# Optimization experiments

Measured on AMD Instinct MI355X. Metric: run time of the kernel, lower is better.

Reference implementation:

```python
import jax, jax.numpy as jnp
import numpy as np

K = 15; P = 3; IN_CH = 128; OUT_CH = 128
NQ_LRF = 4; NS_LRF = 4; LRF_CH = IN_CH // NQ_LRF  # 32
KP_EXTENT = 1.2; RADIUS = 2.5
NQ = 10000; NS = 10000; H = 32


def setup_inputs() -> dict:
    key = jax.random.key(0)
    ks = jax.random.split(key, 10)
    return {
        "q_pts": jax.random.normal(ks[0], (NQ, P), jnp.float32),
        "s_pts": jax.random.normal(ks[1], (NS, P), jnp.float32),
        "neighb_inds": jax.random.randint(ks[2], (NQ, H), 0, NS + 1),  # index NS == shadow point
        "x": jax.random.normal(ks[3], (NS, IN_CH), jnp.float32),
        "q_lrf": jax.random.normal(ks[4], (NQ, NQ_LRF, P, P), jnp.float32),
        "s_lrf": jax.random.normal(ks[5], (NS, NS_LRF, P, P), jnp.float32),
        "weights": jax.random.normal(ks[6], (K, 2 * IN_CH, OUT_CH), jnp.float32) * 0.02,
        "kernel_points": jax.random.normal(ks[7], (K, P), jnp.float32) * (RADIUS * 0.3),
        "mlp_w": jax.random.normal(ks[8], (NS_LRF * P * P, LRF_CH), jnp.float32) * 0.1,
        "mlp_b": jnp.zeros((LRF_CH,), jnp.float32),
    }


def _forward(q_pts, s_pts, neighb_inds, x, q_lrf, s_lrf, weights, kernel_points, mlp_w, mlp_b):
    Nq, Hn = neighb_inds.shape
    Ns = s_pts.shape[0]
    # q_lrf is only ever used detached in the torch module; kernel points are non-trainable
    q_lrf_d = jax.lax.stop_gradient(q_lrf)
    kp = jax.lax.stop_gradient(kernel_points)

    # gather neighbor coords (shadow row at +1e6), center on queries
    s_pts_pad = jnp.concatenate([s_pts, jnp.full((1, P), 1e6, s_pts.dtype)], 0)
    neighbors = s_pts_pad[neighb_inds] - q_pts[:, None, :]            # [Nq,H,3]
    # rotate into each query LRF
    aligned = jnp.einsum('nhd,nqde->nqhe', neighbors, q_lrf_d)        # [Nq,nq,H,3]
    sq_d = jnp.sum((aligned[..., None, :] - kp) ** 2, axis=-1)        # [Nq,nq,H,K]

    # aligned neighbor LRFs: q_lrf^T @ s_lrf_neighbor
    s_lrf_pad = jnp.concatenate([s_lrf, jnp.zeros_like(s_lrf[:1])], 0)
    nb_lrf = s_lrf_pad[neighb_inds]                                   # [Nq,H,ns,3,3]
    aligned_lrf = jnp.einsum('nqba,nhsbc->nhqsac', q_lrf_d, nb_lrf)   # [Nq,H,nq,ns,3,3]
    aligned_lrf = aligned_lrf.reshape(Nq, Hn, NQ_LRF, NS_LRF * P * P)
    lrf_feat = aligned_lrf @ mlp_w + mlp_b                            # [Nq,H,nq,lrf_ch]
    mask = (neighb_inds < Ns).astype(lrf_feat.dtype)                  # shadow-neighbor mask
    lrf_feat = lrf_feat * mask[:, :, None, None]

    # linear kernel-point influence
    all_w = jnp.clip(1.0 - jnp.sqrt(sq_d) / KP_EXTENT, 0.0)           # [Nq,nq,H,K]
    all_w = jnp.swapaxes(all_w, 2, 3)                                 # [Nq,nq,K,H]

    # gather neighbor features (zero shadow row), append lrf features
    x_pad = jnp.concatenate([x.reshape(Ns, NQ_LRF, LRF_CH),
                             jnp.zeros((1, NQ_LRF, LRF_CH), x.dtype)], 0)
    nb_x = x_pad[neighb_inds]                                         # [Nq,H,nq,lc]
    nb_x = jnp.concatenate([nb_x, lrf_feat], axis=-1)                 # [Nq,H,nq,2lc]
    nb_x = jnp.swapaxes(nb_x, 1, 2)                                   # [Nq,nq,H,2lc]

    # influence-weighted aggregation over neighbors, then per-kernel matmul
    wf = jnp.matmul(all_w, nb_x)                                      # [Nq,nq,K,2lc]
    wf = jnp.transpose(wf, (2, 0, 1, 3)).reshape(K, Nq, 2 * IN_CH)    # [K,Nq,fdim]
    return jnp.einsum('knf,kfo->no', wf, weights)                     # [Nq,out]


def reference(q_pts, s_pts, neighb_inds, x, q_lrf, s_lrf, weights, kernel_points, mlp_w, mlp_b):
    return _forward(q_pts, s_pts, neighb_inds, x, q_lrf, s_lrf, weights, kernel_points, mlp_w, mlp_b)
```

## Files before the change

kernel.cpp:

```cpp
#include <hip/hip_runtime.h>

#define NQn 10000
#define NSn 10000
#define Hh  32
#define FDIM 3840

typedef _Float16 f16x8 __attribute__((ext_vector_type(8)));
typedef float    f32x4 __attribute__((ext_vector_type(4)));

__device__ __forceinline__ unsigned pack2h(float a, float b) {
  union { _Float16 h; unsigned short u; } ua, ub;
  ua.h = (_Float16)a; ub.h = (_Float16)b;
  return (unsigned)ua.u | ((unsigned)ub.u << 16);
}

__global__ __launch_bounds__(256) void ekp_prep5(
    const float* __restrict__ w, const float* __restrict__ x,
    _Float16* __restrict__ wt, _Float16* __restrict__ xh)
{
  const int b = blockIdx.x, tid = threadIdx.x;
  if (b < 625) {
    size_t base = (size_t)b*2048 + (size_t)tid*8;
    float4 a0 = *reinterpret_cast<const float4*>(x + base);
    float4 a1 = *reinterpret_cast<const float4*>(x + base + 4);
    uint4 o;
    o.x = pack2h(a0.x, a0.y); o.y = pack2h(a0.z, a0.w);
    o.z = pack2h(a1.x, a1.y); o.w = pack2h(a1.z, a1.w);
    *reinterpret_cast<uint4*>(xh + base) = o;
  } else if (b == 625) {
    if (tid < 64)
      reinterpret_cast<unsigned*>(xh + (size_t)NSn*128)[tid] = 0u;
  } else {
    __shared__ _Float16 t[32][34];
    const int tt = b - 626;
    const int k0 = (tt % 120) * 32, n0 = (tt / 120) * 32;
    const int c = tid & 31, r0 = tid >> 5;
    #pragma unroll
    for (int p = 0; p < 4; ++p) {
      int r = r0 + p*8;
      t[c][r] = (_Float16)w[(size_t)(k0 + r)*128 + n0 + c];
    }
    __syncthreads();
    #pragma unroll
    for (int p = 0; p < 4; ++p) {
      int r = r0 + p*8;
      wt[(size_t)(n0 + r)*FDIM + k0 + c] = t[r][c];
    }
  }
}

__global__ __launch_bounds__(256, 5) void ekp_stage1j(
    const float* __restrict__ q_pts, const float* __restrict__ s_pts,
    const int*   __restrict__ nbi,   const unsigned short* __restrict__ xh,
    const float* __restrict__ q_lrf, const float* __restrict__ s_lrf,
    const float* __restrict__ kp,    const float* __restrict__ mlp_w,
    const float* __restrict__ mlp_b, _Float16* __restrict__ wf_out)
{
  const int n = blockIdx.x;
  const int tid = threadIdx.x;
  const int lane = tid & 63;
  const int wv = tid >> 6;
  const int l15 = lane & 15, lg = lane >> 4;

  __shared__ float sQ[36];
  __shared__ float sMB[32];
  __shared__ int   sIdx[32];
  __shared__ int   sIdxX[32];
  __shared__ float sZ[32];
  __shared__ float sNbr[32][3];
  __shared__ alignas(16) _Float16 sLrfA[32][72];
  __shared__ alignas(16) _Float16 sBw2[4][32][72];
  __shared__ alignas(16) _Float16 sWb[4][16][40];
  #define sFtP(q, m) (&sBw2[q][m][0])

  if (tid < 36) sQ[tid]  = q_lrf[(size_t)n*36 + tid];
  if (tid < 32) sMB[tid] = mlp_b[tid];
  if (tid < 32) {
    int idx = nbi[(size_t)n*Hh + tid];
    int sh = (idx >= NSn) ? 1 : 0;
    sZ[tid]    = sh ? 0.f : 1.f;
    sIdx[tid]  = sh ? 0 : idx;
    sIdxX[tid] = idx;
  }
  { unsigned* z = (unsigned*)&sBw2[0][0][0];
    for (int i = tid; i < 4608; i += 256) z[i] = 0u; }
  { unsigned* z = (unsigned*)&sLrfA[0][0];
    for (int i = tid; i < 1152; i += 256) z[i] = 0u; }
  __syncthreads();

  if (tid < 96) {
    int h = tid / 3, d = tid - h*3;
    sNbr[h][d] = sZ[h] * s_pts[(size_t)sIdx[h]*3 + d] - q_pts[(size_t)n*3 + d];
  }
  for (int f4i = tid; f4i < 288; f4i += 256) {
    int row = f4i / 9, c4 = f4i - row*9;
    float4 v = *reinterpret_cast<const float4*>(
        s_lrf + (size_t)sIdx[row]*36 + c4*4);
    float z = sZ[row];
    uint2 pk;
    pk.x = pack2h(z*v.x, z*v.y);
    pk.y = pack2h(z*v.z, z*v.w);
    *reinterpret_cast<uint2*>(&sLrfA[row][c4*4]) = pk;
  }
  #pragma unroll
  for (int it = 0; it < 18; ++it) {
    int i = tid + it*256;
    int q = i / 1152, r = i - q*1152;
    int k = r >> 5, m = r & 31;
    int s = k / 9, bc = k - s*9, b = bc / 3, c = bc - b*3;
    int br = (s*9 + c)*32 + m;
    float acc = sQ[q*9 + b*3 + 0] * mlp_w[br]
              + sQ[q*9 + b*3 + 1] * mlp_w[br + 96]
              + sQ[q*9 + b*3 + 2] * mlp_w[br + 192];
    sBw2[q][m][k] = (_Float16)acc;
  }
  __syncthreads();

  {
    int h = lane & 31, kh = lane >> 5;
    float a0 = 0.f, a1 = 0.f, a2 = 0.f;
    #pragma unroll
    for (int d = 0; d < 3; ++d) {
      float nd = sNbr[h][d];
      a0 += nd * sQ[wv*9 + d*3 + 0];
      a1 += nd * sQ[wv*9 + d*3 + 1];
      a2 += nd * sQ[wv*9 + d*3 + 2];
    }
    float z = sZ[h];
    int k0 = kh * 8, kend = kh ? 15 : 8;
    for (int k = k0; k < kend; ++k) {
      float d0 = a0 - kp[k*3+0];
      float d1 = a1 - kp[k*3+1];
      float d2 = a2 - kp[k*3+2];
      float wgt = 1.f - sqrtf(d0*d0 + d1*d1 + d2*d2) * (1.0f/1.2f);
      sWb[wv][k][h] = (_Float16)(z * fmaxf(wgt, 0.f));
    }
    if (kh) sWb[wv][15][h] = (_Float16)0.f;
  }
  {
    f32x4 fa[2][2];
    #pragma unroll
    for (int i = 0; i < 2; ++i)
      #pragma unroll
      for (int j = 0; j < 2; ++j) fa[i][j] = (f32x4){0.f,0.f,0.f,0.f};
    #pragma unroll
    for (int kc = 0; kc < 2; ++kc) {
      f16x8 af0 = *reinterpret_cast<const f16x8*>(&sLrfA[l15][kc*32 + lg*8]);
      f16x8 af1 = *reinterpret_cast<const f16x8*>(&sLrfA[16 + l15][kc*32 + lg*8]);
      f16x8 bf0 = *reinterpret_cast<const f16x8*>(&sBw2[wv][l15][kc*32 + lg*8]);
      f16x8 bf1 = *reinterpret_cast<const f16x8*>(&sBw2[wv][16 + l15][kc*32 + lg*8]);
      fa[0][0] = __builtin_amdgcn_mfma_f32_16x16x32_f16(af0, bf0, fa[0][0], 0, 0, 0);
      fa[0][1] = __builtin_amdgcn_mfma_f32_16x16x32_f16(af0, bf1, fa[0][1], 0, 0, 0);
      fa[1][0] = __builtin_amdgcn_mfma_f32_16x16x32_f16(af1, bf0, fa[1][0], 0, 0, 0);
      fa[1][1] = __builtin_amdgcn_mfma_f32_16x16x32_f16(af1, bf1, fa[1][1], 0, 0, 0);
    }
    #pragma unroll
    for (int ht = 0; ht < 2; ++ht) {
      int hb = ht*16 + lg*4;
      float z0 = sZ[hb+0], z1 = sZ[hb+1], z2 = sZ[hb+2], z3 = sZ[hb+3];
      #pragma unroll
      for (int mt = 0; mt < 2; ++mt) {
        int m = mt*16 + l15;
        float bias = sMB[m];
        uint2 pk;
        pk.x = pack2h(fmaf(z0, bias, fa[ht][mt][0]), fmaf(z1, bias, fa[ht][mt][1]));
        pk.y = pack2h(fmaf(z2, bias, fa[ht][mt][2]), fmaf(z3, bias, fa[ht][mt][3]));
        *reinterpret_cast<uint2*>(sFtP(wv, m) + hb) = pk;
      }
    }
  }
  __syncthreads();

  {
    f16x8 a = *reinterpret_cast<const f16x8*>(&sWb[wv][l15][lg*8]);
    union { unsigned u[4]; f16x8 v; } B0, B1;
    #pragma unroll
    for (int j = 0; j < 8; j += 2) {
      int h0 = lg*8 + j, h1 = h0 + 1;
      size_t r0 = (size_t)sIdxX[h0]*128 + wv*32 + l15;
      size_t r1 = (size_t)sIdxX[h1]*128 + wv*32 + l15;
      B0.u[j >> 1] = (unsigned)xh[r0]      | ((unsigned)xh[r1]      << 16);
      B1.u[j >> 1] = (unsigned)xh[r0 + 16] | ((unsigned)xh[r1 + 16] << 16);
    }
    f16x8 b2 = *reinterpret_cast<const f16x8*>(sFtP(wv, l15) + lg*8);
    f16x8 b3 = *reinterpret_cast<const f16x8*>(sFtP(wv, 16 + l15) + lg*8);

    _Float16* wp = wf_out + (size_t)n*FDIM + wv*64 + l15;
    f32x4 acc;
    acc = (f32x4){0.f,0.f,0.f,0.f};
    acc = __builtin_amdgcn_mfma_f32_16x16x32_f16(a, B0.v, acc, 0, 0, 0);
    #pragma unroll
    for (int v = 0; v < 4; ++v) { int k = lg*4 + v; if (k < 15) wp[k*256 +  0] = (_Float16)acc[v]; }
    acc = (f32x4){0.f,0.f,0.f,0.f};
    acc = __builtin_amdgcn_mfma_f32_16x16x32_f16(a, B1.v, acc, 0, 0, 0);
    #pragma unroll
    for (int v = 0; v < 4; ++v) { int k = lg*4 + v; if (k < 15) wp[k*256 + 16] = (_Float16)acc[v]; }
    acc = (f32x4){0.f,0.f,0.f,0.f};
    acc = __builtin_amdgcn_mfma_f32_16x16x32_f16(a, b2, acc, 0, 0, 0);
    #pragma unroll
    for (int v = 0; v < 4; ++v) { int k = lg*4 + v; if (k < 15) wp[k*256 + 32] = (_Float16)acc[v]; }
    acc = (f32x4){0.f,0.f,0.f,0.f};
    acc = __builtin_amdgcn_mfma_f32_16x16x32_f16(a, b3, acc, 0, 0, 0);
    #pragma unroll
    for (int v = 0; v < 4; ++v) { int k = lg*4 + v; if (k < 15) wp[k*256 + 48] = (_Float16)acc[v]; }
  }
  #undef sFtP
}

__global__ __launch_bounds__(256, 4) void ekp_gemm3(
    const _Float16* __restrict__ A,
    const _Float16* __restrict__ Bt,
    float* __restrict__ C)
{
  __shared__ alignas(16) _Float16 As[32][72];
  __shared__ alignas(16) _Float16 Bs[128][72];
  const int tid = threadIdx.x, lane = tid & 63, w = tid >> 6;
  const int wr = w >> 1, wc = w & 1;
  const int r0 = blockIdx.x * 32;
  const int l15 = lane & 15, lg = lane >> 4;

  f32x4 acc[4];
  #pragma unroll
  for (int i = 0; i < 4; ++i) acc[i] = (f32x4){0.f,0.f,0.f,0.f};

  const int sr = tid >> 3;
  const int ak = (tid & 7) << 3;
  const _Float16* ap = A  + (size_t)(r0 + sr)*FDIM + ak;
  const _Float16* bp = Bt + (size_t)sr*FDIM + ak;

  for (int kc = 0; kc < FDIM; kc += 64) {
    *reinterpret_cast<f16x8*>(&As[sr][ak]) = *reinterpret_cast<const f16x8*>(ap + kc);
    #pragma unroll
    for (int p = 0; p < 4; ++p)
      *reinterpret_cast<f16x8*>(&Bs[p*32 + sr][ak]) =
        *reinterpret_cast<const f16x8*>(bp + (size_t)p*32*FDIM + kc);
    __syncthreads();
    #pragma unroll
    for (int k2 = 0; k2 < 2; ++k2) {
      const int ko = k2*32 + lg*8;
      f16x8 a = *reinterpret_cast<const f16x8*>(&As[wr*16 + l15][ko]);
      #pragma unroll
      for (int ni = 0; ni < 4; ++ni) {
        f16x8 b = *reinterpret_cast<const f16x8*>(&Bs[wc*64 + ni*16 + l15][ko]);
        acc[ni] = __builtin_amdgcn_mfma_f32_16x16x32_f16(a, b, acc[ni], 0, 0, 0);
      }
    }
    __syncthreads();
  }
  #pragma unroll
  for (int v = 0; v < 4; ++v) {
    int gr = r0 + wr*16 + lg*4 + v;
    if (gr < NQn) {
      #pragma unroll
      for (int ni = 0; ni < 4; ++ni)
        C[(size_t)gr*128 + wc*64 + ni*16 + l15] = acc[ni][v];
    }
  }
}

__global__ __launch_bounds__(256) void ekp_stage1_fused(
    const float* __restrict__ q_pts, const float* __restrict__ s_pts,
    const int*   __restrict__ nbi,   const float* __restrict__ x,
    const float* __restrict__ q_lrf, const float* __restrict__ s_lrf,
    const float* __restrict__ weights, const float* __restrict__ kp,
    const float* __restrict__ mlp_w, const float* __restrict__ mlp_b,
    float* __restrict__ out)
{
  const int n = blockIdx.x;
  const int tid = threadIdx.x;

  __shared__ float sQ[36];
  __shared__ float sKP[45];
  __shared__ float sMW[36][32];
  __shared__ float sMB[32];
  __shared__ int   sIdx[32];
  __shared__ int   sShad[32];
  __shared__ float sNbr[32][3];
  __shared__ float sLrf[32][37];
  __shared__ float sW[4][15][32];
  __shared__ float sNbx[32][4][65];

  if (tid < 36) sQ[tid]  = q_lrf[(size_t)n*36 + tid];
  if (tid < 45) sKP[tid] = kp[tid];
  if (tid < 32) sMB[tid] = mlp_b[tid];
  for (int i = tid; i < 36*32; i += 256) sMW[i >> 5][i & 31] = mlp_w[i];
  if (tid < 32) {
    int idx = nbi[(size_t)n*Hh + tid];
    int sh = (idx >= NSn) ? 1 : 0;
    sShad[tid] = sh;
    sIdx[tid]  = sh ? 0 : idx;
  }
  __syncthreads();

  if (tid < 96) {
    int h = tid / 3, d = tid - h*3;
    float v = sShad[h] ? 0.f : s_pts[(size_t)sIdx[h]*3 + d];
    sNbr[h][d] = v - q_pts[(size_t)n*3 + d];
  }
  {
    int h = tid >> 3, j0 = tid & 7;
    const float* src = s_lrf + (size_t)sIdx[h]*36;
    float z = sShad[h] ? 0.f : 1.f;
    for (int j = j0; j < 36; j += 8) sLrf[h][j] = z * src[j];
  }
  for (int i = tid; i < Hh*128; i += 256) {
    int h = i >> 7, c = i & 127;
    float v = sShad[h] ? 0.f : x[(size_t)sIdx[h]*128 + c];
    sNbx[h][c >> 5][c & 31] = v;
  }
  __syncthreads();

  {
    int q = tid >> 6, l = tid & 63;
    int h = l & 31, kh = l >> 5;
    float a0 = 0.f, a1 = 0.f, a2 = 0.f;
    #pragma unroll
    for (int d = 0; d < 3; ++d) {
      float nd = sNbr[h][d];
      a0 += nd * sQ[q*9 + d*3 + 0];
      a1 += nd * sQ[q*9 + d*3 + 1];
      a2 += nd * sQ[q*9 + d*3 + 2];
    }
    float z = sShad[h] ? 0.f : 1.f;
    int k0 = kh * 8;
    int kend = k0 + (kh ? 7 : 8);
    for (int k = k0; k < kend; ++k) {
      float d0 = a0 - sKP[k*3+0];
      float d1 = a1 - sKP[k*3+1];
      float d2 = a2 - sKP[k*3+2];
      float wv2 = 1.f - sqrtf(d0*d0 + d1*d1 + d2*d2) * (1.0f/1.2f);
      sW[q][k][h] = z * fmaxf(wv2, 0.f);
    }
  }
  {
    int q = tid >> 6, l = tid & 63;
    int h = l & 31, mh = l >> 5;
    float fi[36];
    #pragma unroll
    for (int s = 0; s < 4; ++s)
      #pragma unroll
      for (int a = 0; a < 3; ++a)
        #pragma unroll
        for (int c = 0; c < 3; ++c) {
          float accv = 0.f;
          #pragma unroll
          for (int b = 0; b < 3; ++b)
            accv += sQ[q*9 + b*3 + a] * sLrf[h][s*9 + b*3 + c];
          fi[s*9 + a*3 + c] = accv;
        }
    float z = sShad[h] ? 0.f : 1.f;
    int m0 = mh * 16;
    for (int mm = 0; mm < 16; ++mm) {
      int m = m0 + mm;
      float accv = sMB[m];
      #pragma unroll
      for (int j = 0; j < 36; ++j) accv += fi[j] * sMW[j][m];
      sNbx[h][q][32 + m] = z * accv;
    }
  }
  __syncthreads();

  float acc[15];
  const int q = tid >> 6, cch = tid & 63;
  #pragma unroll
  for (int k = 0; k < 15; ++k) acc[k] = 0.f;
  for (int h = 0; h < Hh; ++h) {
    float v = sNbx[h][q][cch];
    #pragma unroll
    for (int k = 0; k < 15; ++k) acc[k] += sW[q][k][h] * v;
  }

  __shared__ float sWF[FDIM];
  __shared__ float sRed[2][128];
  #pragma unroll
  for (int k = 0; k < 15; ++k) sWF[k*256 + q*64 + cch] = acc[k];
  __syncthreads();
  int o = tid & 127, part = tid >> 7;
  const float* wp = weights + (size_t)part*1920*128 + o;
  const float* wfp = sWF + part*1920;
  float oa = 0.f;
  #pragma unroll 8
  for (int f = 0; f < 1920; ++f)
    oa += wfp[f] * wp[(size_t)f*128];
  sRed[part][o] = oa;
  __syncthreads();
  if (tid < 128) out[(size_t)n*128 + tid] = sRed[0][tid] + sRed[1][tid];
}

extern "C" void kernel_launch(void* const* d_in, const int* in_sizes, int n_in,
                              void* d_out, int out_size, void* d_ws, size_t ws_size,
                              hipStream_t stream) {
  const float* q_pts   = (const float*)d_in[0];
  const float* s_pts   = (const float*)d_in[1];
  const int*   nbi     = (const int*)  d_in[2];
  const float* x       = (const float*)d_in[3];
  const float* q_lrf   = (const float*)d_in[4];
  const float* s_lrf   = (const float*)d_in[5];
  const float* weights = (const float*)d_in[6];
  const float* kp      = (const float*)d_in[7];
  const float* mlp_w   = (const float*)d_in[8];
  const float* mlp_b   = (const float*)d_in[9];
  float* out = (float*)d_out;

  const size_t nWf = (size_t)NQn * FDIM;
  const size_t nWt = (size_t)128 * FDIM;
  const size_t nXh = (size_t)(NSn + 1) * 128;
  const size_t needBytes = (nWf + nWt + nXh) * sizeof(_Float16);
  if (ws_size >= needBytes) {
    _Float16* wf = (_Float16*)d_ws;
    _Float16* wt = wf + nWf;
    _Float16* xh = wt + nWt;
    ekp_prep5<<<1106, 256, 0, stream>>>(weights, x, wt, xh);
    ekp_stage1j<<<NQn, 256, 0, stream>>>(q_pts, s_pts, nbi,
                                         (const unsigned short*)xh,
                                         q_lrf, s_lrf, kp, mlp_w, mlp_b, wf);
    ekp_gemm3<<<(NQn + 31)/32, 256, 0, stream>>>(wf, wt, out);
  } else {
    ekp_stage1_fused<<<NQn, 256, 0, stream>>>(q_pts, s_pts, nbi, x, q_lrf, s_lrf,
                                              weights, kp, mlp_w, mlp_b, out);
  }
}
```

Before: 133.1 us.

## Split the output GEMM along K into four chunks with a separate reduction kernel

The final fp16 GEMM (10000x128 output, K=3840) is now launched with a second grid dimension of four, so each block covers only a quarter of the K range. Each split writes fp32 partial results to a new workspace buffer, and a new reduce kernel sums the four partials into the output. The aim is to raise block count from about 313 to about 1252, which gives more parallelism and memory-level concurrency on a GPU with many CUs. The cost is extra traffic to write and re-read about 20 MB of partials, plus one more kernel launch.

```diff
diff --git a/kernel.cpp b/kernel.cpp
--- a/kernel.cpp
+++ b/kernel.cpp
@@ -4,6 +4,8 @@
 #define NSn 10000
 #define Hh  32
 #define FDIM 3840
+#define KSPLIT 4
+#define KCHUNK (FDIM / KSPLIT)
 
 typedef _Float16 f16x8 __attribute__((ext_vector_type(8)));
 typedef float    f32x4 __attribute__((ext_vector_type(4)));
@@ -207,16 +209,17 @@
   #undef sFtP
 }
 
-__global__ __launch_bounds__(256, 4) void ekp_gemm3(
+__global__ __launch_bounds__(256, 4) void ekp_gemm5(
     const _Float16* __restrict__ A,
     const _Float16* __restrict__ Bt,
-    float* __restrict__ C)
+    float* __restrict__ Cpart)
 {
   __shared__ alignas(16) _Float16 As[32][72];
   __shared__ alignas(16) _Float16 Bs[128][72];
   const int tid = threadIdx.x, lane = tid & 63, w = tid >> 6;
   const int wr = w >> 1, wc = w & 1;
   const int r0 = blockIdx.x * 32;
+  const int kbase = blockIdx.y * KCHUNK;
   const int l15 = lane & 15, lg = lane >> 4;
 
   f32x4 acc[4];
@@ -228,7 +231,7 @@
   const _Float16* ap = A  + (size_t)(r0 + sr)*FDIM + ak;
   const _Float16* bp = Bt + (size_t)sr*FDIM + ak;
 
-  for (int kc = 0; kc < FDIM; kc += 64) {
+  for (int kc = kbase; kc < kbase + KCHUNK; kc += 64) {
     *reinterpret_cast<f16x8*>(&As[sr][ak]) = *reinterpret_cast<const f16x8*>(ap + kc);
     #pragma unroll
     for (int p = 0; p < 4; ++p)
@@ -247,6 +250,7 @@
     }
     __syncthreads();
   }
+  float* C = Cpart + (size_t)blockIdx.y * NQn * 128;
   #pragma unroll
   for (int v = 0; v < 4; ++v) {
     int gr = r0 + wr*16 + lg*4 + v;
@@ -256,6 +260,21 @@
         C[(size_t)gr*128 + wc*64 + ni*16 + l15] = acc[ni][v];
     }
   }
+}
+
+__global__ __launch_bounds__(256) void ekp_reduce(
+    const float* __restrict__ P, float* __restrict__ out)
+{
+  const size_t i = (size_t)blockIdx.x * 256 + threadIdx.x;
+  const size_t stride = (size_t)NQn * 128 / 4;
+  const float4* p = reinterpret_cast<const float4*>(P);
+  float4 a = p[i], b = p[i + stride], c = p[i + 2*stride], d = p[i + 3*stride];
+  float4 r;
+  r.x = (a.x + b.x) + (c.x + d.x);
+  r.y = (a.y + b.y) + (c.y + d.y);
+  r.z = (a.z + b.z) + (c.z + d.z);
+  r.w = (a.w + b.w) + (c.w + d.w);
+  reinterpret_cast<float4*>(out)[i] = r;
 }
 
 __global__ __launch_bounds__(256) void ekp_stage1_fused(
@@ -405,16 +424,21 @@
   const size_t nWf = (size_t)NQn * FDIM;
   const size_t nWt = (size_t)128 * FDIM;
   const size_t nXh = (size_t)(NSn + 1) * 128;
-  const size_t needBytes = (nWf + nWt + nXh) * sizeof(_Float16);
+  const size_t h16 = nWf + nWt + nXh;
+  const size_t needBytes = h16 * sizeof(_Float16)
+                         + (size_t)KSPLIT * NQn * 128 * sizeof(float);
   if (ws_size >= needBytes) {
     _Float16* wf = (_Float16*)d_ws;
     _Float16* wt = wf + nWf;
     _Float16* xh = wt + nWt;
+    float* cpart = (float*)(xh + nXh);
     ekp_prep5<<<1106, 256, 0, stream>>>(weights, x, wt, xh);
     ekp_stage1j<<<NQn, 256, 0, stream>>>(q_pts, s_pts, nbi,
                                          (const unsigned short*)xh,
                                          q_lrf, s_lrf, kp, mlp_w, mlp_b, wf);
-    ekp_gemm3<<<(NQn + 31)/32, 256, 0, stream>>>(wf, wt, out);
+    dim3 gg((NQn + 31)/32, KSPLIT);
+    ekp_gemm5<<<gg, 256, 0, stream>>>(wf, wt, cpart);
+    ekp_reduce<<<NQn*128/(256*4), 256, 0, stream>>>(cpart, out);
   } else {
     ekp_stage1_fused<<<NQn, 256, 0, stream>>>(q_pts, s_pts, nbi, x, q_lrf, s_lrf,
                                               weights, kp, mlp_w, mlp_b, out);
```

After: 120.0 us. 9.9% less time.
